# Kernel tuning notes

Measured on AMD Instinct MI355X. Metric: run time of the kernel, lower is better.

The kernel has to match this reference:

```python
import jax, jax.numpy as jnp
import numpy as np

EPS = 1e-5

def _sage_conv(x, src, dst, Wl, bl, Wr, num_nodes):
    # PyG SAGEConv (mean aggr): out = lin_l(mean_{j->i} x_j) + lin_r(x_i)
    msg = x[src]                                              # [E, F]
    s = jax.ops.segment_sum(msg, dst, num_segments=num_nodes) # [N, F]
    deg = jax.ops.segment_sum(jnp.ones(src.shape, x.dtype), dst, num_segments=num_nodes)
    mean = s / jnp.maximum(deg, 1.0)[:, None]
    return mean @ Wl + bl + x @ Wr

def _bn(x, gamma, beta):
    # BatchNorm1d in training mode: biased batch statistics
    m = x.mean(axis=0)
    v = x.var(axis=0)
    return (x - m) * jax.lax.rsqrt(v + EPS) * gamma + beta

def setup_inputs() -> dict:
    key = jax.random.key(0)
    ks = jax.random.split(key, 16)
    N, F, H, H1, H2 = 50000, 100, 128, 128, 64
    E = 800000
    def xav(k, fan_in, fan_out):
        lim = float(np.sqrt(6.0 / (fan_in + fan_out)))
        return jax.random.uniform(k, (fan_in, fan_out), jnp.float32, -lim, lim)
    return {
        "x": jax.random.normal(ks[0], (N, F), jnp.float32),
        "edge_index": jax.random.randint(ks[1], (2, E), 0, N, jnp.int32),
        "Wl1": xav(ks[2], F, H), "bl1": jnp.zeros((H,), jnp.float32), "Wr1": xav(ks[3], F, H),
        "Wl2": xav(ks[4], H, H), "bl2": jnp.zeros((H,), jnp.float32), "Wr2": xav(ks[5], H, H),
        "W1": xav(ks[6], H, H1), "b1": jnp.zeros((H1,), jnp.float32),
        "g1": jnp.ones((H1,), jnp.float32), "be1": jnp.zeros((H1,), jnp.float32),
        "W2": xav(ks[7], H1, H2), "b2": jnp.zeros((H2,), jnp.float32),
        "g2": jnp.ones((H2,), jnp.float32), "be2": jnp.zeros((H2,), jnp.float32),
        "W3": xav(ks[8], H2, 1), "b3": jnp.zeros((1,), jnp.float32),
    }

def reference(x, edge_index, Wl1, bl1, Wr1, Wl2, bl2, Wr2,
              W1, b1, g1, be1, W2, b2, g2, be2, W3, b3):
    N = x.shape[0]
    src, dst = edge_index[0], edge_index[1]
    h1 = jax.nn.relu(_sage_conv(x, src, dst, Wl1, bl1, Wr1, N))   # [N, H]
    h2 = jax.nn.relu(_sage_conv(h1, src, dst, Wl2, bl2, Wr2, N))  # [N, H]
    z = jax.nn.relu(_bn(h2 @ W1 + b1, g1, be1))                   # [N, H1]
    z = jax.nn.relu(_bn(z @ W2 + b2, g2, be2))                    # [N, H2]
    out = (z @ W3 + b3).squeeze(-1)                               # [N]
    return out, h1, h2
```

## Files before the change

kernel.cpp:

```cpp
#include <hip/hip_runtime.h>

#define BN_EPS 1e-5f

typedef short s8v __attribute__((ext_vector_type(8)));
typedef float f4v __attribute__((ext_vector_type(4)));
typedef unsigned short u4v __attribute__((ext_vector_type(4)));

__device__ __forceinline__ unsigned short f2bf(float f) {
  union { float f; unsigned u; } v; v.f = f;
  unsigned r = v.u + 0x7FFF + ((v.u >> 16) & 1);
  return (unsigned short)(r >> 16);
}
__device__ __forceinline__ float bf2f(unsigned short u) {
  union { unsigned u; float f; } v; v.u = ((unsigned)u) << 16; return v.f;
}

__global__ __launch_bounds__(256) void deg_kernel(const int* __restrict__ dst,
                                                  int* __restrict__ deg, int E) {
  int e = blockIdx.x * 256 + threadIdx.x;
  if (e < E) atomicAdd(&deg[dst[e]], 1);
}

__global__ __launch_bounds__(256) void scan_partial_kernel(const int* __restrict__ deg,
    int* __restrict__ partials, int N) {
  __shared__ int sh[256];
  int t = threadIdx.x;
  int base = blockIdx.x * 1024 + t * 4;
  int s = 0;
#pragma unroll
  for (int i = 0; i < 4; ++i) {
    int idx = base + i;
    if (idx < N) s += deg[idx];
  }
  sh[t] = s;
  __syncthreads();
  for (int d = 128; d > 0; d >>= 1) {
    if (t < d) sh[t] += sh[t + d];
    __syncthreads();
  }
  if (t == 0) partials[blockIdx.x] = sh[0];
}

__global__ __launch_bounds__(256) void scan_offsets_kernel(const int* __restrict__ partials,
    int* __restrict__ blk_off, int G) {
  __shared__ int sh[256];
  int t = threadIdx.x;
  sh[t] = (t < G) ? partials[t] : 0;
  __syncthreads();
  for (int d = 1; d < 256; d <<= 1) {
    int v = (t >= d) ? sh[t - d] : 0;
    __syncthreads();
    sh[t] += v;
    __syncthreads();
  }
  if (t < G) blk_off[t] = (t == 0) ? 0 : sh[t - 1];
}

__global__ __launch_bounds__(256) void scan_scatter_kernel(const int* __restrict__ deg,
    const int* __restrict__ blk_off, int* __restrict__ row_start,
    int* __restrict__ gcursor, int N) {
  __shared__ int sh[256];
  int t = threadIdx.x;
  int base = blockIdx.x * 1024 + t * 4;
  int v[4];
#pragma unroll
  for (int i = 0; i < 4; ++i) v[i] = (base + i < N) ? deg[base + i] : 0;
  sh[t] = v[0] + v[1] + v[2] + v[3];
  __syncthreads();
  for (int d = 1; d < 256; d <<= 1) {
    int u = (t >= d) ? sh[t - d] : 0;
    __syncthreads();
    sh[t] += u;
    __syncthreads();
  }
  int off = blk_off[blockIdx.x] + ((t == 0) ? 0 : sh[t - 1]);
#pragma unroll
  for (int i = 0; i < 4; ++i) {
    int idx = base + i;
    if (idx < N) {
      row_start[idx] = off;
      if ((idx & 127) == 0) gcursor[idx >> 7] = off;
      off += v[i];
    }
  }
}

#define CHUNK 8192
#define NBMAX 512
__global__ __launch_bounds__(256) void csr_bucket_kernel(
    const int* __restrict__ src, const int* __restrict__ dst,
    int* __restrict__ gcursor, unsigned* __restrict__ pairs, int E) {
  __shared__ int h[NBMAX];
  __shared__ int off[NBMAX];
  __shared__ int cnt2[NBMAX];
  __shared__ int gadj[NBMAX];
  __shared__ unsigned pbuf[CHUNK];
  __shared__ unsigned short bidx[CHUNK];
  int t = threadIdx.x;
  int base = blockIdx.x * CHUNK;
  int cnt = min(CHUNK, E - base);
  for (int i = t; i < NBMAX; i += 256) { h[i] = 0; cnt2[i] = 0; }
  __syncthreads();
  for (int i = t; i < cnt; i += 256) atomicAdd(&h[dst[base + i] >> 7], 1);
  __syncthreads();
  off[t] = h[t]; off[t + 256] = h[t + 256];
  __syncthreads();
  for (int d = 1; d < 512; d <<= 1) {
    int v0 = (t >= d) ? off[t - d] : 0;
    int v1 = off[t + 256 - d];
    __syncthreads();
    off[t] += v0; off[t + 256] += v1;
    __syncthreads();
  }
  int e0 = off[t] - h[t];
  int e1 = off[t + 256] - h[t + 256];
  __syncthreads();
  off[t] = e0; off[t + 256] = e1;
  __syncthreads();
  for (int i = t; i < NBMAX; i += 256) {
    int c = h[i];
    if (c > 0) gadj[i] = atomicAdd(&gcursor[i], c) - off[i];
  }
  __syncthreads();
  for (int i = t; i < cnt; i += 256) {
    int s = src[base + i];
    int d = dst[base + i];
    int b = d >> 7;
    int p = off[b] + atomicAdd(&cnt2[b], 1);
    pbuf[p] = (unsigned)s | ((unsigned)d << 16);
    bidx[p] = (unsigned short)b;
  }
  __syncthreads();
  for (int i = t; i < cnt; i += 256)
    pairs[gadj[bidx[i]] + i] = pbuf[i];
}

__global__ __launch_bounds__(256) void csr_fill_kernel(
    const unsigned* __restrict__ pairs, const int* __restrict__ row_start,
    int* __restrict__ eidx, int N, int E) {
  __shared__ int cur[128];
  int b = blockIdx.x;
  int node0 = b << 7;
  int t = threadIdx.x;
  if (t < 128) {
    int node = node0 + t;
    cur[t] = (node < N) ? row_start[node] : 0;
  }
  __syncthreads();
  int pbeg = row_start[node0];
  int pend = (node0 + 128 < N) ? row_start[node0 + 128] : E;
  for (int i = pbeg + t; i < pend; i += 256) {
    unsigned p = pairs[i];
    int pos = atomicAdd(&cur[(int)(p >> 16) - node0], 1);
    eidx[pos] = (int)(p & 0xFFFFu);
  }
}

__global__ __launch_bounds__(256) void prep_kernel(
    const float* __restrict__ x, unsigned short* __restrict__ xb,
    const float* __restrict__ Wl1, const float* __restrict__ Wr1,
    const float* __restrict__ Wl2, const float* __restrict__ Wr2,
    const float* __restrict__ W1, const float* __restrict__ W2,
    unsigned short* __restrict__ Wl1t, unsigned short* __restrict__ Wr1t,
    unsigned short* __restrict__ Wl2t, unsigned short* __restrict__ Wr2t,
    unsigned short* __restrict__ W1t, unsigned short* __restrict__ W2t,
    int N, int xblocks) {
  int blk = blockIdx.x;
  if (blk < xblocks) {
    int t = blk * 256 + threadIdx.x;
    if (t < N * 128) {
      int col = t & 127;
      int n = t >> 7;
      xb[t] = (col < 100) ? f2bf(x[n * 100 + col]) : (unsigned short)0;
    }
    return;
  }
  int w = blk - xblocks;
  const float* W; unsigned short* Wt; int K, C, base;
  if (w < 64)       { W = Wl1; Wt = Wl1t; K = 100; C = 128; base = 0;   }
  else if (w < 128) { W = Wr1; Wt = Wr1t; K = 100; C = 128; base = 64;  }
  else if (w < 192) { W = Wl2; Wt = Wl2t; K = 128; C = 128; base = 128; }
  else if (w < 256) { W = Wr2; Wt = Wr2t; K = 128; C = 128; base = 192; }
  else if (w < 320) { W = W1;  Wt = W1t;  K = 128; C = 128; base = 256; }
  else              { W = W2;  Wt = W2t;  K = 128; C = 64;  base = 320; }
  int t = (w - base) * 256 + threadIdx.x;
  if (t >= C * 128) return;
  int c = t >> 7;
  int k = t & 127;
  Wt[t] = (k < K) ? f2bf(W[k * C + c]) : (unsigned short)0;
}

__global__ __launch_bounds__(256) void gather_kernel(
    const unsigned short* __restrict__ feat, const int* __restrict__ eidx,
    const int* __restrict__ row_start, const int* __restrict__ deg,
    unsigned short* __restrict__ mean_out, int N) {
  int wave = threadIdx.x >> 6;
  int lane = threadIdx.x & 63;
  int node = blockIdx.x * 4 + wave;
  if (node >= N) return;
  int beg = row_start[node];
  int d = deg[node];
  float a0 = 0.0f, a1 = 0.0f;
  for (int i0 = 0; i0 < d; i0 += 64) {
    int cnt = min(64, d - i0);
    int my = (lane < cnt) ? eidx[beg + i0 + lane] : 0;
    int j = 0;
    for (; j + 7 < cnt; j += 8) {
      int s0 = __shfl(my, j + 0);
      int s1 = __shfl(my, j + 1);
      int s2 = __shfl(my, j + 2);
      int s3 = __shfl(my, j + 3);
      int s4 = __shfl(my, j + 4);
      int s5 = __shfl(my, j + 5);
      int s6 = __shfl(my, j + 6);
      int s7 = __shfl(my, j + 7);
      unsigned v0 = ((const unsigned*)(feat + (size_t)s0 * 128))[lane];
      unsigned v1 = ((const unsigned*)(feat + (size_t)s1 * 128))[lane];
      unsigned v2 = ((const unsigned*)(feat + (size_t)s2 * 128))[lane];
      unsigned v3 = ((const unsigned*)(feat + (size_t)s3 * 128))[lane];
      unsigned v4 = ((const unsigned*)(feat + (size_t)s4 * 128))[lane];
      unsigned v5 = ((const unsigned*)(feat + (size_t)s5 * 128))[lane];
      unsigned v6 = ((const unsigned*)(feat + (size_t)s6 * 128))[lane];
      unsigned v7 = ((const unsigned*)(feat + (size_t)s7 * 128))[lane];
      a0 += bf2f((unsigned short)v0) + bf2f((unsigned short)v1)
          + bf2f((unsigned short)v2) + bf2f((unsigned short)v3)
          + bf2f((unsigned short)v4) + bf2f((unsigned short)v5)
          + bf2f((unsigned short)v6) + bf2f((unsigned short)v7);
      a1 += bf2f((unsigned short)(v0 >> 16)) + bf2f((unsigned short)(v1 >> 16))
          + bf2f((unsigned short)(v2 >> 16)) + bf2f((unsigned short)(v3 >> 16))
          + bf2f((unsigned short)(v4 >> 16)) + bf2f((unsigned short)(v5 >> 16))
          + bf2f((unsigned short)(v6 >> 16)) + bf2f((unsigned short)(v7 >> 16));
    }
    for (; j < cnt; ++j) {
      int s0 = __shfl(my, j);
      unsigned v0 = ((const unsigned*)(feat + (size_t)s0 * 128))[lane];
      a0 += bf2f((unsigned short)v0);
      a1 += bf2f((unsigned short)(v0 >> 16));
    }
  }
  float inv = 1.0f / fmaxf((float)d, 1.0f);
  unsigned o = (unsigned)f2bf(a0 * inv) | ((unsigned)f2bf(a1 * inv) << 16);
  ((unsigned*)(mean_out + (size_t)node * 128))[lane] = o;
}

__global__ __launch_bounds__(128) void bn_prep_kernel(const float* __restrict__ sum,
    const float* __restrict__ sq, const float* __restrict__ g,
    const float* __restrict__ be, float* __restrict__ bnp, int N) {
  int c = threadIdx.x;
  float S = 0.0f, SS = 0.0f;
#pragma unroll
  for (int k = 0; k < 8; ++k) { S += sum[k * 128 + c]; SS += sq[k * 128 + c]; }
  float invN = 1.0f / (float)N;
  float mn = S * invN;
  float var = SS * invN - mn * mn;
  float sc = g[c] * rsqrtf(var + BN_EPS);
  bnp[2 * c] = sc;
  bnp[2 * c + 1] = be[c] - mn * sc;
}

template<int COLS, bool DUAL, bool RELU, bool F32OUT, bool BF16OUT, bool STATS, bool BNIN>
__global__ __launch_bounds__(256, 3) void mfma_gemm_kernel(
    const unsigned short* __restrict__ A1, const unsigned short* __restrict__ W1t,
    const unsigned short* __restrict__ A2, const unsigned short* __restrict__ W2t,
    const float* __restrict__ bias, const float* __restrict__ bnp,
    float* __restrict__ outF, unsigned short* __restrict__ outB,
    float* __restrict__ sum, float* __restrict__ sq, int N) {
  const int CTW = COLS / 64;
  const int CH = COLS / 4;
  __shared__ float lds[64][COLS + 4];
  __shared__ float reds[STATS ? 1024 : 1];
  __shared__ float redq[STATS ? 1024 : 1];
  __shared__ float bnl[BNIN ? 256 : 1];
  int t = threadIdx.x;
  int wave = t >> 6;
  int lane = t & 63;
  int quad = lane >> 4;
  int m = lane & 15;
  int blk = blockIdx.x * 64;
  int col0 = wave * (16 * CTW);

  if (BNIN) {
    bnl[t < 256 ? t : 0] = bnp[t < 256 ? t : 0];
    __syncthreads();
  }

  const unsigned short* a1p[4];
  const unsigned short* a2p[4];
#pragma unroll
  for (int rf = 0; rf < 4; ++rf) {
    int r = blk + rf * 16 + m;
    if (r > N - 1) r = N - 1;
    a1p[rf] = A1 + (size_t)r * 128 + quad * 8;
    if (DUAL) a2p[rf] = A2 + (size_t)r * 128 + quad * 8;
  }

  f4v acc[4][CTW];
#pragma unroll
  for (int rf = 0; rf < 4; ++rf)
#pragma unroll
    for (int ct = 0; ct < CTW; ++ct) acc[rf][ct] = (f4v){0.f, 0.f, 0.f, 0.f};

  s8v a1f[2][4], a2f[2][4];
  s8v B1p[2][CTW], B2p[2][CTW];
#pragma unroll
  for (int rf = 0; rf < 4; ++rf) {
    a1f[0][rf] = *(const s8v*)(a1p[rf]);
    if (DUAL) a2f[0][rf] = *(const s8v*)(a2p[rf]);
  }
#pragma unroll
  for (int ct = 0; ct < CTW; ++ct) {
    size_t wr = (size_t)(col0 + ct * 16 + m) * 128 + quad * 8;
    B1p[0][ct] = *(const s8v*)(W1t + wr);
    if (DUAL) B2p[0][ct] = *(const s8v*)(W2t + wr);
  }

#pragma unroll
  for (int kk = 0; kk < 4; ++kk) {
    const int cur = kk & 1, nxt = cur ^ 1;
    if (kk < 3) {
#pragma unroll
      for (int rf = 0; rf < 4; ++rf) {
        a1f[nxt][rf] = *(const s8v*)(a1p[rf] + (kk + 1) * 32);
        if (DUAL) a2f[nxt][rf] = *(const s8v*)(a2p[rf] + (kk + 1) * 32);
      }
#pragma unroll
      for (int ct = 0; ct < CTW; ++ct) {
        size_t wr = (size_t)(col0 + ct * 16 + m) * 128 + (kk + 1) * 32 + quad * 8;
        B1p[nxt][ct] = *(const s8v*)(W1t + wr);
        if (DUAL) B2p[nxt][ct] = *(const s8v*)(W2t + wr);
      }
    }
    s8v amod[4];
    if (BNIN) {
      float sc[8], sh[8];
#pragma unroll
      for (int i = 0; i < 8; ++i) {
        int c = kk * 32 + quad * 8 + i;
        sc[i] = bnl[2 * c]; sh[i] = bnl[2 * c + 1];
      }
#pragma unroll
      for (int rf = 0; rf < 4; ++rf) {
        s8v raw = a1f[cur][rf];
        s8v a;
#pragma unroll
        for (int i = 0; i < 8; ++i) {
          float v = bf2f((unsigned short)raw[i]);
          v = fmaxf(v * sc[i] + sh[i], 0.0f);
          a[i] = (short)f2bf(v);
        }
        amod[rf] = a;
      }
    }
#pragma unroll
    for (int ct = 0; ct < CTW; ++ct)
#pragma unroll
      for (int rf = 0; rf < 4; ++rf) {
        acc[rf][ct] = __builtin_amdgcn_mfma_f32_16x16x32_bf16(
            BNIN ? amod[rf] : a1f[cur][rf], B1p[cur][ct], acc[rf][ct], 0, 0, 0);
        if (DUAL)
          acc[rf][ct] = __builtin_amdgcn_mfma_f32_16x16x32_bf16(
              a2f[cur][rf], B2p[cur][ct], acc[rf][ct], 0, 0, 0);
      }
  }

#pragma unroll
  for (int ct = 0; ct < CTW; ++ct) {
    int col = col0 + ct * 16 + m;
    float b = bias[col];
#pragma unroll
    for (int rf = 0; rf < 4; ++rf)
#pragma unroll
      for (int r = 0; r < 4; ++r) {
        float v = acc[rf][ct][r] + b;
        if (RELU) v = fmaxf(v, 0.0f);
        lds[rf * 16 + quad * 4 + r][col] = v;
      }
  }
  __syncthreads();
  float s4[4] = {0.f, 0.f, 0.f, 0.f}, q4[4] = {0.f, 0.f, 0.f, 0.f};
  for (int idx = t; idx < 64 * CH; idx += 256) {
    int row = idx / CH;
    int c4 = idx % CH;
    int gr = blk + row;
    if (gr < N) {
      f4v v = *(const f4v*)&lds[row][c4 * 4];
      if (F32OUT) *(f4v*)(outF + (size_t)gr * COLS + c4 * 4) = v;
      if (BF16OUT) {
        u4v o;
#pragma unroll
        for (int j = 0; j < 4; ++j) o[j] = f2bf(v[j]);
        *(u4v*)(outB + (size_t)gr * COLS + c4 * 4) = o;
      }
      if (STATS) {
#pragma unroll
        for (int j = 0; j < 4; ++j) { s4[j] += v[j]; q4[j] += v[j] * v[j]; }
      }
    }
  }
  if (STATS) {
#pragma unroll
    for (int j = 0; j < 4; ++j) { reds[t * 4 + j] = s4[j]; redq[t * 4 + j] = q4[j]; }
    __syncthreads();
    if (t < COLS) {
      int c4 = t >> 2, j = t & 3;
      float S = 0.0f, SS = 0.0f;
#pragma unroll
      for (int g = 0; g < 256 / CH; ++g) {
        S  += reds[(g * CH + c4) * 4 + j];
        SS += redq[(g * CH + c4) * 4 + j];
      }
      int slot = (blockIdx.x & 7) * COLS + t;
      atomicAdd(&sum[slot], S);
      atomicAdd(&sq[slot], SS);
    }
  }
}

__global__ __launch_bounds__(256, 3) void sage_mlp_kernel(
    const unsigned short* __restrict__ A1,
    const unsigned short* __restrict__ Wlt,
    const unsigned short* __restrict__ A2,
    const unsigned short* __restrict__ Wrt,
    const float* __restrict__ bl,
    const unsigned short* __restrict__ W1t, const float* __restrict__ b1,
    float* __restrict__ h2out, unsigned short* __restrict__ y1b,
    float* __restrict__ sum, float* __restrict__ sq, int N) {
  const int RS = 132;
  __shared__ float lds[64 * RS];
  __shared__ float reds[1024];
  __shared__ float redq[1024];
  int t = threadIdx.x;
  int wave = t >> 6, lane = t & 63;
  int quad = lane >> 4, m = lane & 15;
  int blk = blockIdx.x * 64;
  int col0 = wave * 32;

  const unsigned short* a1p[4];
  const unsigned short* a2p[4];
#pragma unroll
  for (int rf = 0; rf < 4; ++rf) {
    int r = blk + rf * 16 + m;
    if (r > N - 1) r = N - 1;
    a1p[rf] = A1 + (size_t)r * 128 + quad * 8;
    a2p[rf] = A2 + (size_t)r * 128 + quad * 8;
  }
  f4v acc[4][2];
#pragma unroll
  for (int rf = 0; rf < 4; ++rf)
#pragma unroll
    for (int ct = 0; ct < 2; ++ct) acc[rf][ct] = (f4v){0.f, 0.f, 0.f, 0.f};

  s8v a1f[2][4], a2f[2][4];
  s8v BLp[2][2], BRp[2][2];
#pragma unroll
  for (int rf = 0; rf < 4; ++rf) {
    a1f[0][rf] = *(const s8v*)(a1p[rf]);
    a2f[0][rf] = *(const s8v*)(a2p[rf]);
  }
#pragma unroll
  for (int ct = 0; ct < 2; ++ct) {
    size_t wr = (size_t)(col0 + ct * 16 + m) * 128 + quad * 8;
    BLp[0][ct] = *(const s8v*)(Wlt + wr);
    BRp[0][ct] = *(const s8v*)(Wrt + wr);
  }
#pragma unroll
  for (int kk = 0; kk < 4; ++kk) {
    const int cur = kk & 1, nxt = cur ^ 1;
    if (kk < 3) {
#pragma unroll
      for (int rf = 0; rf < 4; ++rf) {
        a1f[nxt][rf] = *(const s8v*)(a1p[rf] + (kk + 1) * 32);
        a2f[nxt][rf] = *(const s8v*)(a2p[rf] + (kk + 1) * 32);
      }
#pragma unroll
      for (int ct = 0; ct < 2; ++ct) {
        size_t wr = (size_t)(col0 + ct * 16 + m) * 128 + (kk + 1) * 32 + quad * 8;
        BLp[nxt][ct] = *(const s8v*)(Wlt + wr);
        BRp[nxt][ct] = *(const s8v*)(Wrt + wr);
      }
    }
#pragma unroll
    for (int ct = 0; ct < 2; ++ct)
#pragma unroll
      for (int rf = 0; rf < 4; ++rf) {
        acc[rf][ct] = __builtin_amdgcn_mfma_f32_16x16x32_bf16(a1f[cur][rf], BLp[cur][ct], acc[rf][ct], 0, 0, 0);
        acc[rf][ct] = __builtin_amdgcn_mfma_f32_16x16x32_bf16(a2f[cur][rf], BRp[cur][ct], acc[rf][ct], 0, 0, 0);
      }
  }

  s8v bw[2][8];
#pragma unroll
  for (int ct = 0; ct < 8; ++ct)
    bw[0][ct] = *(const s8v*)(W1t + (size_t)(ct * 16 + m) * 128 + quad * 8);

#pragma unroll
  for (int ct = 0; ct < 2; ++ct) {
    int col = col0 + ct * 16 + m;
    float b = bl[col];
#pragma unroll
    for (int rf = 0; rf < 4; ++rf)
#pragma unroll
      for (int r = 0; r < 4; ++r)
        lds[(rf * 16 + quad * 4 + r) * RS + col] = fmaxf(acc[rf][ct][r] + b, 0.0f);
  }
  __syncthreads();

  for (int idx = t; idx < 64 * 32; idx += 256) {
    int row = idx >> 5;
    int c4 = idx & 31;
    int gr = blk + row;
    if (gr < N)
      *(f4v*)(h2out + (size_t)gr * 128 + c4 * 4) = *(const f4v*)&lds[row * RS + c4 * 4];
  }

  int arow = wave * 16 + m;
  s8v af[4];
#pragma unroll
  for (int kk = 0; kk < 4; ++kk) {
    int k0 = kk * 32 + quad * 8;
    f4v x0 = *(const f4v*)&lds[arow * RS + k0];
    f4v x1 = *(const f4v*)&lds[arow * RS + k0 + 4];
    s8v a;
#pragma unroll
    for (int i = 0; i < 4; ++i) { a[i] = (short)f2bf(x0[i]); a[4 + i] = (short)f2bf(x1[i]); }
    af[kk] = a;
  }

  f4v acc2[8];
#pragma unroll
  for (int ct = 0; ct < 8; ++ct) acc2[ct] = (f4v){0.f, 0.f, 0.f, 0.f};
#pragma unroll
  for (int kk = 0; kk < 4; ++kk) {
    const int cur = kk & 1, nxt = cur ^ 1;
    if (kk < 3) {
#pragma unroll
      for (int ct = 0; ct < 8; ++ct)
        bw[nxt][ct] = *(const s8v*)(W1t + (size_t)(ct * 16 + m) * 128 + (kk + 1) * 32 + quad * 8);
    }
#pragma unroll
    for (int ct = 0; ct < 8; ++ct)
      acc2[ct] = __builtin_amdgcn_mfma_f32_16x16x32_bf16(af[kk], bw[cur][ct], acc2[ct], 0, 0, 0);
  }
  __syncthreads();
#pragma unroll
  for (int ct = 0; ct < 8; ++ct) {
    int col = ct * 16 + m;
    float b = b1[col];
#pragma unroll
    for (int r = 0; r < 4; ++r)
      lds[(wave * 16 + quad * 4 + r) * RS + col] = acc2[ct][r] + b;
  }
  __syncthreads();

  float s4[4] = {0.f, 0.f, 0.f, 0.f}, q4[4] = {0.f, 0.f, 0.f, 0.f};
  for (int idx = t; idx < 64 * 32; idx += 256) {
    int row = idx >> 5;
    int c4 = idx & 31;
    int gr = blk + row;
    if (gr < N) {
      f4v v = *(const f4v*)&lds[row * RS + c4 * 4];
      u4v o;
#pragma unroll
      for (int j = 0; j < 4; ++j) o[j] = f2bf(v[j]);
      *(u4v*)(y1b + (size_t)gr * 128 + c4 * 4) = o;
#pragma unroll
      for (int j = 0; j < 4; ++j) { s4[j] += v[j]; q4[j] += v[j] * v[j]; }
    }
  }
#pragma unroll
  for (int j = 0; j < 4; ++j) { reds[t * 4 + j] = s4[j]; redq[t * 4 + j] = q4[j]; }
  __syncthreads();
  if (t < 128) {
    int c4 = t >> 2, j = t & 3;
    float S = 0.0f, SS = 0.0f;
#pragma unroll
    for (int g = 0; g < 8; ++g) {
      S  += reds[(g * 32 + c4) * 4 + j];
      SS += redq[(g * 32 + c4) * 4 + j];
    }
    int slot = (blockIdx.x & 7) * 128 + t;
    atomicAdd(&sum[slot], S);
    atomicAdd(&sq[slot], SS);
  }
}

__global__ __launch_bounds__(256) void bn_head_kernel(const float* __restrict__ y2,
    const float* __restrict__ sum, const float* __restrict__ sumsq,
    const float* __restrict__ g, const float* __restrict__ be,
    const float* __restrict__ W3, const float* __restrict__ b3,
    float* __restrict__ out, int N) {
  int wave = threadIdx.x >> 6;
  int lane = threadIdx.x & 63;
  int row = blockIdx.x * 4 + wave;
  if (row >= N) return;
  float S = 0.0f, SS = 0.0f;
#pragma unroll
  for (int k = 0; k < 8; ++k) { S += sum[k * 64 + lane]; SS += sumsq[k * 64 + lane]; }
  float invN = 1.0f / (float)N;
  float m = S * invN;
  float var = SS * invN - m * m;
  float val = (y2[(size_t)row * 64 + lane] - m) * rsqrtf(var + BN_EPS) * g[lane] + be[lane];
  val = fmaxf(val, 0.0f) * W3[lane];
#pragma unroll
  for (int off = 32; off > 0; off >>= 1) val += __shfl_down(val, off);
  if (lane == 0) out[row] = val + b3[0];
}

extern "C" void kernel_launch(void* const* d_in, const int* in_sizes, int n_in,
                              void* d_out, int out_size, void* d_ws, size_t ws_size,
                              hipStream_t stream) {
  const int F = 100, H = 128;
  const int N = in_sizes[0] / F;
  const int E = in_sizes[1] / 2;

  const float* x   = (const float*)d_in[0];
  const int* edge  = (const int*)d_in[1];
  const int* src   = edge;
  const int* dst   = edge + E;
  const float* Wl1 = (const float*)d_in[2];
  const float* bl1 = (const float*)d_in[3];
  const float* Wr1 = (const float*)d_in[4];
  const float* Wl2 = (const float*)d_in[5];
  const float* bl2 = (const float*)d_in[6];
  const float* Wr2 = (const float*)d_in[7];
  const float* W1  = (const float*)d_in[8];
  const float* b1  = (const float*)d_in[9];
  const float* g1  = (const float*)d_in[10];
  const float* be1 = (const float*)d_in[11];
  const float* W2  = (const float*)d_in[12];
  const float* b2  = (const float*)d_in[13];
  const float* g2  = (const float*)d_in[14];
  const float* be2 = (const float*)d_in[15];
  const float* W3  = (const float*)d_in[16];
  const float* b3  = (const float*)d_in[17];

  float* out0 = (float*)d_out;
  float* h1   = out0 + N;
  float* h2   = h1 + (size_t)N * H;

  const int SCAN_G = (N + 1023) / 1024;
  const int NB = (N + 127) / 128;

  char* wsp = (char*)d_ws;
  int* deg       = (int*)wsp;               wsp += (size_t)N * sizeof(int);
  int* row_start = (int*)wsp;               wsp += (size_t)N * sizeof(int);
  int* eidx      = (int*)wsp;               wsp += (size_t)E * sizeof(int);
  unsigned* pairs = (unsigned*)wsp;         wsp += (size_t)E * sizeof(unsigned);
  int* gcursor   = (int*)wsp;               wsp += 512 * sizeof(int);
  int* partials  = (int*)wsp;               wsp += 256 * sizeof(int);
  int* blk_off   = (int*)wsp;               wsp += 256 * sizeof(int);
  float* sum1    = (float*)wsp;             wsp += 8 * 128 * sizeof(float);
  float* sq1     = (float*)wsp;             wsp += 8 * 128 * sizeof(float);
  float* sum2    = (float*)wsp;             wsp += 8 * 64 * sizeof(float);
  float* sq2     = (float*)wsp;             wsp += 8 * 64 * sizeof(float);
  float* bnp     = (float*)wsp;             wsp += 256 * sizeof(float);
  float* bufA    = (float*)wsp;             wsp += (size_t)N * 128 * sizeof(float);
  unsigned short* bfX = (unsigned short*)wsp; wsp += (size_t)N * 128 * 2;
  unsigned short* bfM = (unsigned short*)wsp; wsp += (size_t)N * 128 * 2;
  unsigned short* bfH = (unsigned short*)wsp; wsp += (size_t)N * 128 * 2;
  unsigned short* Wl1t = (unsigned short*)wsp; wsp += 128 * 128 * 2;
  unsigned short* Wr1t = (unsigned short*)wsp; wsp += 128 * 128 * 2;
  unsigned short* Wl2t = (unsigned short*)wsp; wsp += 128 * 128 * 2;
  unsigned short* Wr2t = (unsigned short*)wsp; wsp += 128 * 128 * 2;
  unsigned short* W1t  = (unsigned short*)wsp; wsp += 128 * 128 * 2;
  unsigned short* W2t  = (unsigned short*)wsp; wsp += 64 * 128 * 2;

  unsigned short* y1b = (unsigned short*)bufA;
  float* y2 = (float*)((char*)bufA + (size_t)N * 128 * 2);

  hipMemsetAsync(deg, 0, (size_t)N * sizeof(int), stream);
  hipMemsetAsync(sum1, 0, (8 * 128 + 8 * 128 + 8 * 64 + 8 * 64) * sizeof(float), stream);

  deg_kernel<<<(E + 255) / 256, 256, 0, stream>>>(dst, deg, E);
  scan_partial_kernel<<<SCAN_G, 256, 0, stream>>>(deg, partials, N);
  scan_offsets_kernel<<<1, 256, 0, stream>>>(partials, blk_off, SCAN_G);
  scan_scatter_kernel<<<SCAN_G, 256, 0, stream>>>(deg, blk_off, row_start, gcursor, N);
  csr_bucket_kernel<<<(E + CHUNK - 1) / CHUNK, 256, 0, stream>>>(src, dst, gcursor, pairs, E);
  csr_fill_kernel<<<NB, 256, 0, stream>>>(pairs, row_start, eidx, N, E);

  int xblocks = ((size_t)N * 128 + 255) / 256;
  prep_kernel<<<xblocks + 352, 256, 0, stream>>>(x, bfX,
      Wl1, Wr1, Wl2, Wr2, W1, W2, Wl1t, Wr1t, Wl2t, Wr2t, W1t, W2t, N, xblocks);

  int gemm_grid = (N + 63) / 64;

  gather_kernel<<<(N + 3) / 4, 256, 0, stream>>>(bfX, eidx, row_start, deg, bfM, N);
  mfma_gemm_kernel<128, true, true, true, true, false, false><<<gemm_grid, 256, 0, stream>>>(
      bfM, Wl1t, bfX, Wr1t, bl1, nullptr, h1, bfH, nullptr, nullptr, N);

  gather_kernel<<<(N + 3) / 4, 256, 0, stream>>>(bfH, eidx, row_start, deg, bfM, N);
  sage_mlp_kernel<<<gemm_grid, 256, 0, stream>>>(
      bfM, Wl2t, bfH, Wr2t, bl2, W1t, b1, h2, y1b, sum1, sq1, N);

  bn_prep_kernel<<<1, 128, 0, stream>>>(sum1, sq1, g1, be1, bnp, N);

  mfma_gemm_kernel<64, false, false, true, false, true, true><<<gemm_grid, 256, 0, stream>>>(
      y1b, W2t, nullptr, nullptr, b2, bnp, y2, nullptr, sum2, sq2, N);

  bn_head_kernel<<<(N + 3) / 4, 256, 0, stream>>>(
      y2, sum2, sq2, g2, be2, W3, b3, out0, N);
}
```

Before: 351.8 us.

## Halve GEMM row tiles, stage A through swizzled LDS, preload weights

Both MFMA GEMM kernels and the fused SAGE+MLP kernel now process 32-row tiles instead of 64, and the grid doubles to match. Each block loads its A rows with coalesced 16-byte loads into an XOR-swizzled LDS buffer, replacing strided per-lane global fragment loads. All weight fragments for the block's columns are preloaded into registers up front. The second GEMM in the fused kernel is re-split so each wave owns a column slice across all 32 rows. The aim is better memory coalescing and more resident blocks (launch bounds raised to 4 blocks per CU). In exchange, each weight fragment is reloaded by twice as many blocks, and the last tile reads past row N without clamping.

Measured after the change: 323.5 us. -8.0%, faster.

```diff
diff --git a/kernel.cpp b/kernel.cpp
--- a/kernel.cpp
+++ b/kernel.cpp
@@ -259,78 +259,82 @@
 }
 
 template<int COLS, bool DUAL, bool RELU, bool F32OUT, bool BF16OUT, bool STATS, bool BNIN>
-__global__ __launch_bounds__(256, 3) void mfma_gemm_kernel(
+__global__ __launch_bounds__(256, 4) void mfma_gemm_kernel(
     const unsigned short* __restrict__ A1, const unsigned short* __restrict__ W1t,
     const unsigned short* __restrict__ A2, const unsigned short* __restrict__ W2t,
     const float* __restrict__ bias, const float* __restrict__ bnp,
     float* __restrict__ outF, unsigned short* __restrict__ outB,
     float* __restrict__ sum, float* __restrict__ sq, int N) {
-  const int CTW = COLS / 64;
-  const int CH = COLS / 4;
-  __shared__ float lds[64][COLS + 4];
-  __shared__ float reds[STATS ? 1024 : 1];
-  __shared__ float redq[STATS ? 1024 : 1];
-  __shared__ float bnl[BNIN ? 256 : 1];
+  constexpr int CTW = COLS / 64;
+  constexpr int CH = COLS / 4;
+  constexpr int RS = COLS + 4;
+  constexpr int NA = DUAL ? 2 : 1;
+  constexpr int OUT_OFF = 8192 * NA;
+  constexpr int BNL_OFF = OUT_OFF + 32 * RS * 4;
+  constexpr int SMEM_SZ = BNL_OFF + (BNIN ? 1024 : 0);
+  __shared__ char smem[SMEM_SZ];
+  float* outl = (float*)(smem + OUT_OFF);
+  float* reds = (float*)smem;
+  float* redq = (float*)(smem + 4096);
+  float* bnl  = (float*)(smem + BNL_OFF);
   int t = threadIdx.x;
   int wave = t >> 6;
   int lane = t & 63;
   int quad = lane >> 4;
   int m = lane & 15;
-  int blk = blockIdx.x * 64;
+  int blk = blockIdx.x * 32;
   int col0 = wave * (16 * CTW);
 
-  if (BNIN) {
-    bnl[t < 256 ? t : 0] = bnp[t < 256 ? t : 0];
-    __syncthreads();
-  }
-
-  const unsigned short* a1p[4];
-  const unsigned short* a2p[4];
-#pragma unroll
-  for (int rf = 0; rf < 4; ++rf) {
-    int r = blk + rf * 16 + m;
-    if (r > N - 1) r = N - 1;
-    a1p[rf] = A1 + (size_t)r * 128 + quad * 8;
-    if (DUAL) a2p[rf] = A2 + (size_t)r * 128 + quad * 8;
-  }
-
-  f4v acc[4][CTW];
-#pragma unroll
-  for (int rf = 0; rf < 4; ++rf)
+  if (BNIN) bnl[t] = bnp[t];
+
+  s8v B1r[4][CTW], B2r[4][CTW];
+  {
+    int c0 = wave * 2, c1 = c0 + 1;
+    const char* g1 = (const char*)A1 + (size_t)blk * 256;
+    s8v va = *(const s8v*)(g1 + c0 * 1024 + lane * 16);
+    s8v vb = *(const s8v*)(g1 + c1 * 1024 + lane * 16);
+    s8v vc, vd;
+    if (DUAL) {
+      const char* g2 = (const char*)A2 + (size_t)blk * 256;
+      vc = *(const s8v*)(g2 + c0 * 1024 + lane * 16);
+      vd = *(const s8v*)(g2 + c1 * 1024 + lane * 16);
+    }
+#pragma unroll
+    for (int kk = 0; kk < 4; ++kk)
+#pragma unroll
+      for (int ct = 0; ct < CTW; ++ct) {
+        size_t wr = (size_t)(col0 + ct * 16 + m) * 128 + kk * 32 + quad * 8;
+        B1r[kk][ct] = *(const s8v*)(W1t + wr);
+        if (DUAL) B2r[kk][ct] = *(const s8v*)(W2t + wr);
+      }
+    int r0 = c0 * 4 + (lane >> 4);
+    int r1 = r0 + 4;
+    int cb = (lane & 15) << 4;
+    *(s8v*)(smem + r0 * 256 + (cb ^ ((r0 & 7) << 4))) = va;
+    *(s8v*)(smem + r1 * 256 + (cb ^ ((r1 & 7) << 4))) = vb;
+    if (DUAL) {
+      *(s8v*)(smem + 8192 + r0 * 256 + (cb ^ ((r0 & 7) << 4))) = vc;
+      *(s8v*)(smem + 8192 + r1 * 256 + (cb ^ ((r1 & 7) << 4))) = vd;
+    }
+  }
+  __syncthreads();
+
+  f4v acc[2][CTW];
+#pragma unroll
+  for (int rf = 0; rf < 2; ++rf)
 #pragma unroll
     for (int ct = 0; ct < CTW; ++ct) acc[rf][ct] = (f4v){0.f, 0.f, 0.f, 0.f};
-
-  s8v a1f[2][4], a2f[2][4];
-  s8v B1p[2][CTW], B2p[2][CTW];
-#pragma unroll
-  for (int rf = 0; rf < 4; ++rf) {
-    a1f[0][rf] = *(const s8v*)(a1p[rf]);
-    if (DUAL) a2f[0][rf] = *(const s8v*)(a2p[rf]);
-  }
-#pragma unroll
-  for (int ct = 0; ct < CTW; ++ct) {
-    size_t wr = (size_t)(col0 + ct * 16 + m) * 128 + quad * 8;
-    B1p[0][ct] = *(const s8v*)(W1t + wr);
-    if (DUAL) B2p[0][ct] = *(const s8v*)(W2t + wr);
-  }
-
 #pragma unroll
   for (int kk = 0; kk < 4; ++kk) {
-    const int cur = kk & 1, nxt = cur ^ 1;
-    if (kk < 3) {
-#pragma unroll
-      for (int rf = 0; rf < 4; ++rf) {
-        a1f[nxt][rf] = *(const s8v*)(a1p[rf] + (kk + 1) * 32);
-        if (DUAL) a2f[nxt][rf] = *(const s8v*)(a2p[rf] + (kk + 1) * 32);
-      }
-#pragma unroll
-      for (int ct = 0; ct < CTW; ++ct) {
-        size_t wr = (size_t)(col0 + ct * 16 + m) * 128 + (kk + 1) * 32 + quad * 8;
-        B1p[nxt][ct] = *(const s8v*)(W1t + wr);
-        if (DUAL) B2p[nxt][ct] = *(const s8v*)(W2t + wr);
-      }
-    }
-    s8v amod[4];
+    int cb2 = kk * 64 + quad * 16;
+    s8v a1[2], a2[2];
+#pragma unroll
+    for (int rf = 0; rf < 2; ++rf) {
+      int rr = rf * 16 + m;
+      int sw = rr * 256 + (cb2 ^ ((rr & 7) << 4));
+      a1[rf] = *(const s8v*)(smem + sw);
+      if (DUAL) a2[rf] = *(const s8v*)(smem + 8192 + sw);
+    }
     if (BNIN) {
       float sc[8], sh[8];
 #pragma unroll
@@ -339,8 +343,8 @@
         sc[i] = bnl[2 * c]; sh[i] = bnl[2 * c + 1];
       }
 #pragma unroll
-      for (int rf = 0; rf < 4; ++rf) {
-        s8v raw = a1f[cur][rf];
+      for (int rf = 0; rf < 2; ++rf) {
+        s8v raw = a1[rf];
         s8v a;
 #pragma unroll
         for (int i = 0; i < 8; ++i) {
@@ -348,18 +352,16 @@
           v = fmaxf(v * sc[i] + sh[i], 0.0f);
           a[i] = (short)f2bf(v);
         }
-        amod[rf] = a;
+        a1[rf] = a;
       }
     }
 #pragma unroll
     for (int ct = 0; ct < CTW; ++ct)
 #pragma unroll
-      for (int rf = 0; rf < 4; ++rf) {
-        acc[rf][ct] = __builtin_amdgcn_mfma_f32_16x16x32_bf16(
-            BNIN ? amod[rf] : a1f[cur][rf], B1p[cur][ct], acc[rf][ct], 0, 0, 0);
+      for (int rf = 0; rf < 2; ++rf) {
+        acc[rf][ct] = __builtin_amdgcn_mfma_f32_16x16x32_bf16(a1[rf], B1r[kk][ct], acc[rf][ct], 0, 0, 0);
         if (DUAL)
-          acc[rf][ct] = __builtin_amdgcn_mfma_f32_16x16x32_bf16(
-              a2f[cur][rf], B2p[cur][ct], acc[rf][ct], 0, 0, 0);
+          acc[rf][ct] = __builtin_amdgcn_mfma_f32_16x16x32_bf16(a2[rf], B2r[kk][ct], acc[rf][ct], 0, 0, 0);
       }
   }
 
@@ -368,22 +370,22 @@
     int col = col0 + ct * 16 + m;
     float b = bias[col];
 #pragma unroll
-    for (int rf = 0; rf < 4; ++rf)
+    for (int rf = 0; rf < 2; ++rf)
 #pragma unroll
       for (int r = 0; r < 4; ++r) {
         float v = acc[rf][ct][r] + b;
         if (RELU) v = fmaxf(v, 0.0f);
-        lds[rf * 16 + quad * 4 + r][col] = v;
+        outl[(rf * 16 + quad * 4 + r) * RS + col] = v;
       }
   }
   __syncthreads();
   float s4[4] = {0.f, 0.f, 0.f, 0.f}, q4[4] = {0.f, 0.f, 0.f, 0.f};
-  for (int idx = t; idx < 64 * CH; idx += 256) {
+  for (int idx = t; idx < 32 * CH; idx += 256) {
     int row = idx / CH;
     int c4 = idx % CH;
     int gr = blk + row;
     if (gr < N) {
-      f4v v = *(const f4v*)&lds[row][c4 * 4];
+      f4v v = *(const f4v*)&outl[row * RS + c4 * 4];
       if (F32OUT) *(f4v*)(outF + (size_t)gr * COLS + c4 * 4) = v;
       if (BF16OUT) {
         u4v o;
@@ -398,6 +400,7 @@
     }
   }
   if (STATS) {
+    __syncthreads();
 #pragma unroll
     for (int j = 0; j < 4; ++j) { reds[t * 4 + j] = s4[j]; redq[t * 4 + j] = q4[j]; }
     __syncthreads();
@@ -416,7 +419,7 @@
   }
 }
 
-__global__ __launch_bounds__(256, 3) void sage_mlp_kernel(
+__global__ __launch_bounds__(256, 4) void sage_mlp_kernel(
     const unsigned short* __restrict__ A1,
     const unsigned short* __restrict__ Wlt,
     const unsigned short* __restrict__ A2,
@@ -425,140 +428,143 @@
     const unsigned short* __restrict__ W1t, const float* __restrict__ b1,
     float* __restrict__ h2out, unsigned short* __restrict__ y1b,
     float* __restrict__ sum, float* __restrict__ sq, int N) {
-  const int RS = 132;
-  __shared__ float lds[64 * RS];
-  __shared__ float reds[1024];
-  __shared__ float redq[1024];
+  constexpr int RS = 132;
+  constexpr int OUT_OFF = 16384;
+  __shared__ char smem[OUT_OFF + 32 * RS * 4];
+  float* outl = (float*)(smem + OUT_OFF);
+  float* reds = (float*)smem;
+  float* redq = (float*)(smem + 4096);
   int t = threadIdx.x;
   int wave = t >> 6, lane = t & 63;
   int quad = lane >> 4, m = lane & 15;
-  int blk = blockIdx.x * 64;
+  int blk = blockIdx.x * 32;
   int col0 = wave * 32;
 
-  const unsigned short* a1p[4];
-  const unsigned short* a2p[4];
-#pragma unroll
-  for (int rf = 0; rf < 4; ++rf) {
-    int r = blk + rf * 16 + m;
-    if (r > N - 1) r = N - 1;
-    a1p[rf] = A1 + (size_t)r * 128 + quad * 8;
-    a2p[rf] = A2 + (size_t)r * 128 + quad * 8;
-  }
-  f4v acc[4][2];
-#pragma unroll
-  for (int rf = 0; rf < 4; ++rf)
+  s8v BLr[4][2], BRr[4][2];
+  {
+    int c0 = wave * 2, c1 = c0 + 1;
+    const char* g1 = (const char*)A1 + (size_t)blk * 256;
+    const char* g2 = (const char*)A2 + (size_t)blk * 256;
+    s8v va = *(const s8v*)(g1 + c0 * 1024 + lane * 16);
+    s8v vb = *(const s8v*)(g1 + c1 * 1024 + lane * 16);
+    s8v vc = *(const s8v*)(g2 + c0 * 1024 + lane * 16);
+    s8v vd = *(const s8v*)(g2 + c1 * 1024 + lane * 16);
+#pragma unroll
+    for (int kk = 0; kk < 4; ++kk)
+#pragma unroll
+      for (int ct = 0; ct < 2; ++ct) {
+        size_t wr = (size_t)(col0 + ct * 16 + m) * 128 + kk * 32 + quad * 8;
+        BLr[kk][ct] = *(const s8v*)(Wlt + wr);
+        BRr[kk][ct] = *(const s8v*)(Wrt + wr);
+      }
+    int r0 = c0 * 4 + (lane >> 4);
+    int r1 = r0 + 4;
+    int cb = (lane & 15) << 4;
+    *(s8v*)(smem + r0 * 256 + (cb ^ ((r0 & 7) << 4))) = va;
+    *(s8v*)(smem + r1 * 256 + (cb ^ ((r1 & 7) << 4))) = vb;
+    *(s8v*)(smem + 8192 + r0 * 256 + (cb ^ ((r0 & 7) << 4))) = vc;
+    *(s8v*)(smem + 8192 + r1 * 256 + (cb ^ ((r1 & 7) << 4))) = vd;
+  }
+  __syncthreads();
+
+  f4v acc[2][2];
+#pragma unroll
+  for (int rf = 0; rf < 2; ++rf)
 #pragma unroll
     for (int ct = 0; ct < 2; ++ct) acc[rf][ct] = (f4v){0.f, 0.f, 0.f, 0.f};
-
-  s8v a1f[2][4], a2f[2][4];
-  s8v BLp[2][2], BRp[2][2];
-#pragma unroll
-  for (int rf = 0; rf < 4; ++rf) {
-    a1f[0][rf] = *(const s8v*)(a1p[rf]);
-    a2f[0][rf] = *(const s8v*)(a2p[rf]);
-  }
-#pragma unroll
-  for (int ct = 0; ct < 2; ++ct) {
-    size_t wr = (size_t)(col0 + ct * 16 + m) * 128 + quad * 8;
-    BLp[0][ct] = *(const s8v*)(Wlt + wr);
-    BRp[0][ct] = *(const s8v*)(Wrt + wr);
-  }
 #pragma unroll
   for (int kk = 0; kk < 4; ++kk) {
-    const int cur = kk & 1, nxt = cur ^ 1;
-    if (kk < 3) {
-#pragma unroll
-      for (int rf = 0; rf < 4; ++rf) {
-        a1f[nxt][rf] = *(const s8v*)(a1p[rf] + (kk + 1) * 32);
-        a2f[nxt][rf] = *(const s8v*)(a2p[rf] + (kk + 1) * 32);
-      }
-#pragma unroll
-      for (int ct = 0; ct < 2; ++ct) {
-        size_t wr = (size_t)(col0 + ct * 16 + m) * 128 + (kk + 1) * 32 + quad * 8;
-        BLp[nxt][ct] = *(const s8v*)(Wlt + wr);
-        BRp[nxt][ct] = *(const s8v*)(Wrt + wr);
-      }
+    int cb2 = kk * 64 + quad * 16;
+    s8v a1[2], a2[2];
+#pragma unroll
+    for (int rf = 0; rf < 2; ++rf) {
+      int rr = rf * 16 + m;
+      int sw = rr * 256 + (cb2 ^ ((rr & 7) << 4));
+      a1[rf] = *(const s8v*)(smem + sw);
+      a2[rf] = *(const s8v*)(smem + 8192 + sw);
     }
 #pragma unroll
     for (int ct = 0; ct < 2; ++ct)
 #pragma unroll
-      for (int rf = 0; rf < 4; ++rf) {
-        acc[rf][ct] = __builtin_amdgcn_mfma_f32_16x16x32_bf16(a1f[cur][rf], BLp[cur][ct], acc[rf][ct], 0, 0, 0);
-        acc[rf][ct] = __builtin_amdgcn_mfma_f32_16x16x32_bf16(a2f[cur][rf], BRp[cur][ct], acc[rf][ct], 0, 0, 0);
-      }
-  }
-
-  s8v bw[2][8];
-#pragma unroll
-  for (int ct = 0; ct < 8; ++ct)
-    bw[0][ct] = *(const s8v*)(W1t + (size_t)(ct * 16 + m) * 128 + quad * 8);
+      for (int rf = 0; rf < 2; ++rf) {
+        acc[rf][ct] = __builtin_amdgcn_mfma_f32_16x16x32_bf16(a1[rf], BLr[kk][ct], acc[rf][ct], 0, 0, 0);
+        acc[rf][ct] = __builtin_amdgcn_mfma_f32_16x16x32_bf16(a2[rf], BRr[kk][ct], acc[rf][ct], 0, 0, 0);
+      }
+  }
+
+  s8v bw[4][2];
+#pragma unroll
+  for (int kk = 0; kk < 4; ++kk)
+#pragma unroll
+    for (int ct = 0; ct < 2; ++ct)
+      bw[kk][ct] = *(const s8v*)(W1t + (size_t)(col0 + ct * 16 + m) * 128 + kk * 32 + quad * 8);
 
 #pragma unroll
   for (int ct = 0; ct < 2; ++ct) {
     int col = col0 + ct * 16 + m;
     float b = bl[col];
 #pragma unroll
-    for (int rf = 0; rf < 4; ++rf)
+    for (int rf = 0; rf < 2; ++rf)
 #pragma unroll
       for (int r = 0; r < 4; ++r)
-        lds[(rf * 16 + quad * 4 + r) * RS + col] = fmaxf(acc[rf][ct][r] + b, 0.0f);
-  }
-  __syncthreads();
-
-  for (int idx = t; idx < 64 * 32; idx += 256) {
+        outl[(rf * 16 + quad * 4 + r) * RS + col] = fmaxf(acc[rf][ct][r] + b, 0.0f);
+  }
+  __syncthreads();
+
+  for (int idx = t; idx < 32 * 32; idx += 256) {
     int row = idx >> 5;
     int c4 = idx & 31;
     int gr = blk + row;
     if (gr < N)
-      *(f4v*)(h2out + (size_t)gr * 128 + c4 * 4) = *(const f4v*)&lds[row * RS + c4 * 4];
-  }
-
-  int arow = wave * 16 + m;
-  s8v af[4];
-#pragma unroll
-  for (int kk = 0; kk < 4; ++kk) {
-    int k0 = kk * 32 + quad * 8;
-    f4v x0 = *(const f4v*)&lds[arow * RS + k0];
-    f4v x1 = *(const f4v*)&lds[arow * RS + k0 + 4];
-    s8v a;
-#pragma unroll
-    for (int i = 0; i < 4; ++i) { a[i] = (short)f2bf(x0[i]); a[4 + i] = (short)f2bf(x1[i]); }
-    af[kk] = a;
-  }
-
-  f4v acc2[8];
-#pragma unroll
-  for (int ct = 0; ct < 8; ++ct) acc2[ct] = (f4v){0.f, 0.f, 0.f, 0.f};
-#pragma unroll
-  for (int kk = 0; kk < 4; ++kk) {
-    const int cur = kk & 1, nxt = cur ^ 1;
-    if (kk < 3) {
-#pragma unroll
-      for (int ct = 0; ct < 8; ++ct)
-        bw[nxt][ct] = *(const s8v*)(W1t + (size_t)(ct * 16 + m) * 128 + (kk + 1) * 32 + quad * 8);
-    }
-#pragma unroll
-    for (int ct = 0; ct < 8; ++ct)
-      acc2[ct] = __builtin_amdgcn_mfma_f32_16x16x32_bf16(af[kk], bw[cur][ct], acc2[ct], 0, 0, 0);
-  }
-  __syncthreads();
-#pragma unroll
-  for (int ct = 0; ct < 8; ++ct) {
-    int col = ct * 16 + m;
+      *(f4v*)(h2out + (size_t)gr * 128 + c4 * 4) = *(const f4v*)&outl[row * RS + c4 * 4];
+  }
+
+  s8v af[2][4];
+#pragma unroll
+  for (int rf = 0; rf < 2; ++rf)
+#pragma unroll
+    for (int kk = 0; kk < 4; ++kk) {
+      int k0 = kk * 32 + quad * 8;
+      f4v x0 = *(const f4v*)&outl[(rf * 16 + m) * RS + k0];
+      f4v x1 = *(const f4v*)&outl[(rf * 16 + m) * RS + k0 + 4];
+      s8v a;
+#pragma unroll
+      for (int i = 0; i < 4; ++i) { a[i] = (short)f2bf(x0[i]); a[4 + i] = (short)f2bf(x1[i]); }
+      af[rf][kk] = a;
+    }
+
+  f4v acc2[2][2];
+#pragma unroll
+  for (int rf = 0; rf < 2; ++rf)
+#pragma unroll
+    for (int ct = 0; ct < 2; ++ct) acc2[rf][ct] = (f4v){0.f, 0.f, 0.f, 0.f};
+#pragma unroll
+  for (int kk = 0; kk < 4; ++kk)
+#pragma unroll
+    for (int ct = 0; ct < 2; ++ct)
+#pragma unroll
+      for (int rf = 0; rf < 2; ++rf)
+        acc2[rf][ct] = __builtin_amdgcn_mfma_f32_16x16x32_bf16(af[rf][kk], bw[kk][ct], acc2[rf][ct], 0, 0, 0);
+  __syncthreads();
+#pragma unroll
+  for (int ct = 0; ct < 2; ++ct) {
+    int col = col0 + ct * 16 + m;
     float b = b1[col];
 #pragma unroll
-    for (int r = 0; r < 4; ++r)
-      lds[(wave * 16 + quad * 4 + r) * RS + col] = acc2[ct][r] + b;
+    for (int rf = 0; rf < 2; ++rf)
+#pragma unroll
+      for (int r = 0; r < 4; ++r)
+        outl[(rf * 16 + quad * 4 + r) * RS + col] = acc2[rf][ct][r] + b;
   }
   __syncthreads();
 
   float s4[4] = {0.f, 0.f, 0.f, 0.f}, q4[4] = {0.f, 0.f, 0.f, 0.f};
-  for (int idx = t; idx < 64 * 32; idx += 256) {
+  for (int idx = t; idx < 32 * 32; idx += 256) {
     int row = idx >> 5;
     int c4 = idx & 31;
     int gr = blk + row;
     if (gr < N) {
-      f4v v = *(const f4v*)&lds[row * RS + c4 * 4];
+      f4v v = *(const f4v*)&outl[row * RS + c4 * 4];
       u4v o;
 #pragma unroll
       for (int j = 0; j < 4; ++j) o[j] = f2bf(v[j]);
@@ -682,7 +688,7 @@
   prep_kernel<<<xblocks + 352, 256, 0, stream>>>(x, bfX,
       Wl1, Wr1, Wl2, Wr2, W1, W2, Wl1t, Wr1t, Wl2t, Wr2t, W1t, W2t, N, xblocks);
 
-  int gemm_grid = (N + 63) / 64;
+  int gemm_grid = (N + 31) / 32;
 
   gather_kernel<<<(N + 3) / 4, 256, 0, stream>>>(bfX, eidx, row_start, deg, bfM, N);
   mfma_gemm_kernel<128, true, true, true, true, false, false><<<gemm_grid, 256, 0, stream>>>(
```
